# Optimization experiments

Measured on AMD Instinct MI355X. Metric: run time of the kernel, lower is better.

Reference implementation:

```python
import jax, jax.numpy as jnp
import numpy as np

B = 4096
N = 8192
LEVEL_SIZES = [8, 128, 2048, 6008]  # sums to N; 4-level taxonomy
EPS = 1e-07


def _build_hierarchy():
    """parent[c] = parent node index (-1 for roots); level_of[c] = depth."""
    rng = np.random.default_rng(0)
    parent = np.full(N, -1, np.int32)
    level_of = np.zeros(N, np.int32)
    off, prev_start, prev_size = 0, 0, 0
    for l, sz in enumerate(LEVEL_SIZES):
        level_of[off:off + sz] = l
        if l > 0:
            parent[off:off + sz] = rng.integers(prev_start, prev_start + prev_size, sz)
        prev_start, prev_size = off, sz
        off += sz
    return parent, level_of


def setup_inputs() -> dict:
    key = jax.random.key(0)
    k1, k2 = jax.random.split(key)
    pred = jax.random.normal(k1, (B, N), dtype=jnp.float32)  # logits
    target = (jax.random.uniform(k2, (B, N)) < 0.02).astype(jnp.float32)
    parent_np, level_np = _build_hierarchy()
    return {
        "pred": pred,
        "target": target,
        "parent": jnp.asarray(parent_np),
        "level_of": jnp.asarray(level_np),
        "mode": 0,  # 0 = EVAL (propagate conditional probs), 1 = TRAIN
    }


def reference(pred, target, parent, level_of, mode):
    p = jax.nn.sigmoid(pred)                      # [B, N]
    parent_clip = jnp.maximum(parent, 0)          # safe gather index for roots
    is_root = parent < 0                          # recursive_relation[-1]

    if mode != 1:  # not 'TRAIN': top-down conditional probability propagation
        pc = p
        for l in range(1, len(LEVEL_SIZES)):
            # pred_clone[:, children(n)] = pred[:, children] * pred_clone[:, n]
            pc = jnp.where(level_of == l, p * pc[:, parent_clip], pc)
        pred_clone = pc
    else:
        pred_clone = None

    # mask[b, c] = 1 if c is a root, or if target[b, parent[c]] == 1
    mask = jnp.where(is_root, jnp.float32(1.0), target[:, parent_clip])

    pcl = jnp.clip(p, EPS, 1.0 - EPS)
    loss = -(jnp.log(pcl) * target + (1.0 - target) * mask * jnp.log(1.0 - pcl))
    loss = loss.sum(axis=1).mean()
    return (loss, pred_clone)
```

## Files before the change

kernel.cpp:

```cpp
#include <hip/hip_runtime.h>


#define N_NODES 8192
#define L1S 8
#define L2S 136
#define L3S 2184
#define N4   (N_NODES / 4)
#define L3S4 (L3S / 4)
#define NA 3
#define NB 6
#define NF 9

__device__ __forceinline__ float frcp(float x) { return __builtin_amdgcn_rcpf(x); }

__global__ __launch_bounds__(256, 4) void cs_main(
    const float* __restrict__ pred,
    const float* __restrict__ target,
    const int* __restrict__ parent,
    float* __restrict__ out,
    float* __restrict__ bsum,
    float inv_b)
{
    __shared__ float pk[L3S];
    __shared__ float red[4];

    const int tid = threadIdx.x;
    const int b = blockIdx.x;
    const float* __restrict__ prow = pred + (size_t)b * N_NODES;
    const float* __restrict__ trow = target + (size_t)b * N_NODES;
    float* __restrict__ orow = out + 1 + (size_t)b * N_NODES;

    float4 ax[NA], atg[NA];
#pragma unroll
    for (int k = 0; k < NA; ++k) {
        const int g = min(tid + k * 256, L3S4 - 1);
        ax[k]  = ((const float4*)prow)[g];
        atg[k] = ((const float4*)trow)[g];
    }
    float4 bx[NB], btg[NB]; int4 bq[NB];
#pragma unroll
    for (int k = 0; k < NB; ++k) {
        const int g = min(L3S4 + tid + k * 256, N4 - 1);
        bx[k]  = ((const float4*)prow)[g];
        btg[k] = ((const float4*)trow)[g];
        bq[k]  = ((const int4*)parent)[g];
    }

#pragma unroll
    for (int k = 0; k < NA; ++k) {
        const int g = tid + k * 256;
        if (g < L3S4) {
            const float xs[4] = {ax[k].x, ax[k].y, ax[k].z, ax[k].w};
            const float ts[4] = {atg[k].x, atg[k].y, atg[k].z, atg[k].w};
            const int c0 = g * 4;
#pragma unroll
            for (int j = 0; j < 4; ++j) {
                const float p = frcp(1.0f + __expf(-xs[j]));
                pk[c0 + j] = ts[j] > 0.5f ? -p : p;
            }
        }
    }

    int q1[NF], q2[NF];
#pragma unroll
    for (int k = 0; k < NF; ++k) {
        const int c = min(tid + k * 256, L3S - 1);
        q1[k] = parent[c];
    }
#pragma unroll
    for (int k = 0; k < NF; ++k) {
        q2[k] = parent[max(q1[k], 0)];
    }
    __syncthreads();

    float lsum = 0.0f;
#pragma unroll
    for (int k = 0; k < NF; ++k) {
        const int c = tid + k * 256;
        if (c < L3S) {
            const float v = pk[c];
            const float p = fabsf(v);
            const bool t = (v < 0.0f);
            float mask, cum;
            if (c < L1S) {
                mask = 1.0f; cum = p;
            } else {
                const float pv = pk[q1[k]];
                mask = (pv < 0.0f) ? 1.0f : 0.0f;
                if (c < L2S) {
                    cum = p * fabsf(pv);
                } else {
                    const float gv = pk[q2[k]];
                    cum = p * fabsf(pv) * fabsf(gv);
                    pk[c] = t ? -cum : cum;
                }
            }
            lsum += t ? -__logf(p) : mask * (-__logf(1.0f - p));
            orow[c] = cum;
        }
    }
    __syncthreads();

#pragma unroll
    for (int k = 0; k < NB; ++k) {
        const int g = L3S4 + tid + k * 256;
        if (g < N4) {
            const float xs[4] = {bx[k].x, bx[k].y, bx[k].z, bx[k].w};
            const float ts[4] = {btg[k].x, btg[k].y, btg[k].z, btg[k].w};
            const int   qs[4] = {bq[k].x, bq[k].y, bq[k].z, bq[k].w};
            float r[4];
#pragma unroll
            for (int j = 0; j < 4; ++j) {
                const float x = xs[j], t = ts[j];
                const float pv = pk[qs[j]];
                const float mask = (pv < 0.0f) ? 1.0f : 0.0f;
                const float e = __expf(-x);
                const float s = __logf(1.0f + e);
                const float p = frcp(1.0f + e);
                lsum += t * s + (1.0f - t) * mask * (s + x);
                r[j] = p * fabsf(pv);
            }
            const int c0 = g * 4;
            orow[c0] = r[0];
            *(float2*)(orow + c0 + 1) = make_float2(r[1], r[2]);
            orow[c0 + 3] = r[3];
        }
    }

#pragma unroll
    for (int off = 32; off > 0; off >>= 1) lsum += __shfl_down(lsum, off);
    if ((tid & 63) == 0) red[tid >> 6] = lsum;
    __syncthreads();
    if (tid == 0) {
        const float s = (red[0] + red[1]) + (red[2] + red[3]);
        if (bsum) bsum[blockIdx.x] = s;
        else atomicAdd(out, s * inv_b);
    }
}

__global__ __launch_bounds__(256) void cs_finish(
    const float* __restrict__ bsum, float* __restrict__ out,
    int nblocks, float inv_b)
{
    __shared__ float red[4];
    const int tid = threadIdx.x;
    float s = 0.0f;
    for (int i = tid; i < nblocks; i += 256) s += bsum[i];
#pragma unroll
    for (int off = 32; off > 0; off >>= 1) s += __shfl_down(s, off);
    if ((tid & 63) == 0) red[tid >> 6] = s;
    __syncthreads();
    if (tid == 0) out[0] = ((red[0] + red[1]) + (red[2] + red[3])) * inv_b;
}

extern "C" void kernel_launch(void* const* d_in, const int* in_sizes, int n_in,
                              void* d_out, int out_size, void* d_ws, size_t ws_size,
                              hipStream_t stream) {
    const float* pred   = (const float*)d_in[0];
    const float* target = (const float*)d_in[1];
    const int*   parent = (const int*)d_in[2];

    float* out = (float*)d_out;
    const int batch = in_sizes[0] / N_NODES;
    const float inv_b = 1.0f / (float)batch;

    if (ws_size >= (size_t)batch * sizeof(float)) {
        float* bsum = (float*)d_ws;
        cs_main<<<batch, 256, 0, stream>>>(pred, target, parent, out, bsum, inv_b);
        cs_finish<<<1, 256, 0, stream>>>(bsum, out, batch, inv_b);
    } else {
        hipMemsetAsync(d_out, 0, sizeof(float), stream);
        cs_main<<<batch, 256, 0, stream>>>(pred, target, parent, out, nullptr, inv_b);
    }
}
```

Before: 89.02 us.

## Stream level-4 loads with register double-buffering and aligned shuffled float4 stores

```diff
diff --git a/kernel.cpp b/kernel.cpp
--- a/kernel.cpp
+++ b/kernel.cpp
@@ -1,19 +1,22 @@
 #include <hip/hip_runtime.h>
 
+
+typedef float f4 __attribute__((ext_vector_type(4)));
+typedef float f2 __attribute__((ext_vector_type(2)));
+typedef int   i4 __attribute__((ext_vector_type(4)));
 
 #define N_NODES 8192
 #define L1S 8
 #define L2S 136
 #define L3S 2184
-#define N4   (N_NODES / 4)
-#define L3S4 (L3S / 4)
+#define N4   2048
+#define L3S4 546
 #define NA 3
 #define NB 6
-#define NF 9
 
 __device__ __forceinline__ float frcp(float x) { return __builtin_amdgcn_rcpf(x); }
 
-__global__ __launch_bounds__(256, 4) void cs_main(
+__global__ __launch_bounds__(256, 8) void cs_main(
     const float* __restrict__ pred,
     const float* __restrict__ target,
     const int* __restrict__ parent,
@@ -28,54 +31,39 @@
     const int b = blockIdx.x;
     const float* __restrict__ prow = pred + (size_t)b * N_NODES;
     const float* __restrict__ trow = target + (size_t)b * N_NODES;
-    float* __restrict__ orow = out + 1 + (size_t)b * N_NODES;
+    float* __restrict__ obase = out + (size_t)b * N_NODES;
 
-    float4 ax[NA], atg[NA];
+    f4 ax[NA], at[NA];
 #pragma unroll
     for (int k = 0; k < NA; ++k) {
         const int g = min(tid + k * 256, L3S4 - 1);
-        ax[k]  = ((const float4*)prow)[g];
-        atg[k] = ((const float4*)trow)[g];
-    }
-    float4 bx[NB], btg[NB]; int4 bq[NB];
-#pragma unroll
-    for (int k = 0; k < NB; ++k) {
-        const int g = min(L3S4 + tid + k * 256, N4 - 1);
-        bx[k]  = ((const float4*)prow)[g];
-        btg[k] = ((const float4*)trow)[g];
-        bq[k]  = ((const int4*)parent)[g];
+        ax[k] = ((const f4*)prow)[g];
+        at[k] = ((const f4*)trow)[g];
     }
 
 #pragma unroll
     for (int k = 0; k < NA; ++k) {
         const int g = tid + k * 256;
         if (g < L3S4) {
-            const float xs[4] = {ax[k].x, ax[k].y, ax[k].z, ax[k].w};
-            const float ts[4] = {atg[k].x, atg[k].y, atg[k].z, atg[k].w};
             const int c0 = g * 4;
 #pragma unroll
             for (int j = 0; j < 4; ++j) {
-                const float p = frcp(1.0f + __expf(-xs[j]));
-                pk[c0 + j] = ts[j] > 0.5f ? -p : p;
+                const float p = frcp(1.0f + __expf(-ax[k][j]));
+                pk[c0 + j] = at[k][j] > 0.5f ? -p : p;
             }
         }
     }
 
-    int q1[NF], q2[NF];
-#pragma unroll
-    for (int k = 0; k < NF; ++k) {
-        const int c = min(tid + k * 256, L3S - 1);
-        q1[k] = parent[c];
-    }
-#pragma unroll
-    for (int k = 0; k < NF; ++k) {
-        q2[k] = parent[max(q1[k], 0)];
-    }
+    int g = L3S4 + tid;
+    f4 x4 = ((const f4*)prow)[g];
+    f4 t4 = ((const f4*)trow)[g];
+    i4 q4 = ((const i4*)parent)[g];
+
     __syncthreads();
 
     float lsum = 0.0f;
 #pragma unroll
-    for (int k = 0; k < NF; ++k) {
+    for (int k = 0; k < 9; ++k) {
         const int c = tid + k * 256;
         if (c < L3S) {
             const float v = pk[c];
@@ -85,46 +73,62 @@
             if (c < L1S) {
                 mask = 1.0f; cum = p;
             } else {
-                const float pv = pk[q1[k]];
+                const int pa = parent[c];
+                const float pv = pk[pa];
                 mask = (pv < 0.0f) ? 1.0f : 0.0f;
                 if (c < L2S) {
                     cum = p * fabsf(pv);
                 } else {
-                    const float gv = pk[q2[k]];
+                    const float gv = pk[parent[pa]];
                     cum = p * fabsf(pv) * fabsf(gv);
                     pk[c] = t ? -cum : cum;
                 }
             }
             lsum += t ? -__logf(p) : mask * (-__logf(1.0f - p));
-            orow[c] = cum;
+            __builtin_nontemporal_store(cum, obase + c + 1);
         }
     }
     __syncthreads();
 
+    const int lane = tid & 63;
 #pragma unroll
     for (int k = 0; k < NB; ++k) {
-        const int g = L3S4 + tid + k * 256;
+        f4 nx, ntg; i4 nq;
+        if (k + 1 < NB) {
+            const int gi = min(g + 256, N4 - 1);
+            nx  = ((const f4*)prow)[gi];
+            ntg = ((const f4*)trow)[gi];
+            nq  = ((const i4*)parent)[gi];
+        }
+        float rr[4];
+#pragma unroll
+        for (int j = 0; j < 4; ++j) {
+            const float x = x4[j], t = t4[j];
+            const float pv = pk[q4[j]];
+            const float mask = (pv < 0.0f) ? 1.0f : 0.0f;
+            const float e = __expf(-x);
+            const float s = __logf(1.0f + e);
+            const float p = frcp(1.0f + e);
+            const float le = t * s + (1.0f - t) * mask * (s + x);
+            lsum += (g < N4) ? le : 0.0f;
+            rr[j] = p * fabsf(pv);
+        }
+        const float prev3 = __shfl_up(rr[3], 1);
         if (g < N4) {
-            const float xs[4] = {bx[k].x, bx[k].y, bx[k].z, bx[k].w};
-            const float ts[4] = {btg[k].x, btg[k].y, btg[k].z, btg[k].w};
-            const int   qs[4] = {bq[k].x, bq[k].y, bq[k].z, bq[k].w};
-            float r[4];
-#pragma unroll
-            for (int j = 0; j < 4; ++j) {
-                const float x = xs[j], t = ts[j];
-                const float pv = pk[qs[j]];
-                const float mask = (pv < 0.0f) ? 1.0f : 0.0f;
-                const float e = __expf(-x);
-                const float s = __logf(1.0f + e);
-                const float p = frcp(1.0f + e);
-                lsum += t * s + (1.0f - t) * mask * (s + x);
-                r[j] = p * fabsf(pv);
+            float* slot = obase + 4 * g;
+            if (lane > 0) {
+                f4 v = {prev3, rr[0], rr[1], rr[2]};
+                __builtin_nontemporal_store(v, (f4*)slot);
+            } else {
+                __builtin_nontemporal_store(rr[0], slot + 1);
+                f2 v2 = {rr[1], rr[2]};
+                __builtin_nontemporal_store(v2, (f2*)(slot + 2));
             }
-            const int c0 = g * 4;
-            orow[c0] = r[0];
-            *(float2*)(orow + c0 + 1) = make_float2(r[1], r[2]);
-            orow[c0 + 3] = r[3];
+            if (lane == 63 || g == N4 - 1) {
+                __builtin_nontemporal_store(rr[3], slot + 4);
+            }
         }
+        x4 = nx; t4 = ntg; q4 = nq; g += 256;
     }
 
 #pragma unroll
```

Measured after the change: 147.9 us. +66.2%, slower.
